# Kernel optimization log

Measured on AMD Instinct MI355X. Metric: run time of the kernel, lower is better.

Reference implementation:

```python
import jax, jax.numpy as jnp
import numpy as np

EPS = 1e-12

def _l2norm(x):
    # F.normalize(p=2, dim=1) with eps clamp on the norm
    n = jnp.linalg.norm(x, axis=1, keepdims=True)
    return x / jnp.maximum(n, EPS)

def _xavier_uniform(key, shape, gain=1.414):
    fan_in, fan_out = shape[-1], shape[0]
    a = gain * np.sqrt(6.0 / (fan_in + fan_out))
    return jax.random.uniform(key, shape, jnp.float32, -a, a)

def setup_inputs() -> dict:
    NUM_ENT, NUM_REL, D, E, B = 100000, 500, 512, 150000, 4096
    key = jax.random.key(0)
    ks = jax.random.split(key, 12)
    heads = jax.random.randint(ks[0], (B, 1), 0, NUM_ENT)
    rels  = jax.random.randint(ks[1], (B, 1), 0, NUM_REL)
    tails = jax.random.randint(ks[2], (B, 1), 0, NUM_ENT)
    triples = jnp.concatenate([heads, rels, tails], axis=1)           # [B,3]
    node_list = jax.random.randint(ks[3], (2, E), 0, NUM_ENT)          # [2,E] (src,dst)
    edge_list = jax.random.randint(ks[4], (E,), 0, NUM_REL)            # [E] relation per edge
    return {
        "triples": triples,
        "node_list": node_list,
        "edge_list": edge_list,
        "ent_emb_init": jax.random.normal(ks[5], (NUM_ENT, D), jnp.float32),
        "rel_emb_init": jax.random.normal(ks[6], (NUM_REL, D), jnp.float32),
        "W_1": _xavier_uniform(ks[7], (D, D)),
        "W_a": _xavier_uniform(ks[8], (1, D)),
        "g_0": _xavier_uniform(ks[9], (1, D)),
        "W_E": _xavier_uniform(ks[10], (D, D)),
        "W_R": _xavier_uniform(ks[11], (D, D)),
    }

def reference(triples, node_list, edge_list, ent_emb_init, rel_emb_init,
              W_1, W_a, g_0, W_E, W_R):
    num_ent = ent_emb_init.shape[0]
    e0 = _l2norm(ent_emb_init)                      # normalized entity table [N,D]
    src, dst = node_list[0], node_list[1]
    h_i = e0[src]                                   # [E,D]
    h_j = e0[dst]                                   # [E,D]
    g_k = rel_emb_init[edge_list]                   # [E,D]

    # c_ijk = W_1 @ (h_j*g_k)^T  -> kept edge-major as [E,D]
    c = (h_j * g_k) @ W_1.T                         # [E,D]
    a = -jax.nn.leaky_relu((h_i * jnp.tanh(c)) @ W_a[0], 0.2)   # [E]
    c_base = (h_i * g_0) @ W_1.T                    # [E,D]
    a_base = -jax.nn.leaky_relu((h_i * jnp.tanh(c_base)) @ W_a[0], 0.2)  # [E]

    a_exp = jnp.exp(a)                              # [E]
    ab_exp = jnp.exp(a_base)                        # [E]

    # segment-softmax denominator: sum of edge exps per source node + baseline term
    a_exp_sum = jax.ops.segment_sum(a_exp[:, None], src, num_segments=num_ent)  # [N,1]
    # baseline exp depends only on src node -> duplicate scatter-set writes identical values
    ab_sorted = jnp.zeros_like(a_exp_sum).at[src].set(ab_exp[:, None])           # [N,1]
    denom = ab_sorted + a_exp_sum
    denom = jnp.where(denom == 0.0, EPS, denom)

    # weighted scatter-aggregate of messages (dropout omitted: eval-mode identity)
    ac = a_exp[:, None] * c                         # [E,D]
    ac_base = ab_exp[:, None] * c_base              # [E,D]
    a_new = jax.ops.segment_sum(ac, src, num_segments=num_ent)                   # [N,D]
    ab_new = jnp.zeros_like(a_new).at[src].set(ac_base)                          # [N,D]

    h_prime = jax.nn.elu((ab_new + a_new) / denom)  # [N,D]
    ent_new = _l2norm(e0 @ W_E + h_prime)           # [N,D]
    rel_new = rel_emb_init @ W_R                    # [R,D]

    head = ent_new[triples[:, 0]][:, None, :]       # [B,1,D]
    rel  = rel_new[triples[:, 1]][:, None, :]       # [B,1,D]
    tail = ent_new[triples[:, 2]][:, None, :]       # [B,1,D]
    return jnp.concatenate([head, rel, tail], axis=1)  # [B,3,D]
```

## Files before the change

### kernel.cpp

```cpp
#include <hip/hip_runtime.h>
#include <cmath>


#define DDIM 512
#define MAXM 65536
#define GBM 128
#define GBN 128

typedef __attribute__((ext_vector_type(8))) short short8;
typedef __attribute__((ext_vector_type(4))) short short4v;
typedef __attribute__((ext_vector_type(4))) float fv4;
typedef unsigned short u16;
typedef unsigned long long u64;

#define LOG2E 1.4426950408889634f

__device__ __forceinline__ float fast_tanh(float x) {
    x = fminf(fmaxf(x, -30.f), 30.f);
    float e = __builtin_amdgcn_exp2f(2.f * LOG2E * x);
    return (e - 1.f) * __builtin_amdgcn_rcpf(e + 1.f);
}
__device__ __forceinline__ float fast_elu(float x) {
    return x > 0.f ? x : (__builtin_amdgcn_exp2f(LOG2E * x) - 1.f);
}
__device__ __forceinline__ float sexp(float x) {
    float lr = x >= 0.f ? x : 0.2f * x;
    return expf(-lr);
}
__device__ __forceinline__ u16 f2bf(float x) {
    unsigned u = __float_as_uint(x);
    u += 0x7FFFu + ((u >> 16) & 1u);
    return (u16)(u >> 16);
}
__device__ __forceinline__ float bf2f(u16 h) {
    return __uint_as_float((unsigned)h << 16);
}
__device__ __forceinline__ void cvt8(const float* v, short8& h8, short8& l8) {
    #pragma unroll
    for (int i = 0; i < 8; i++) {
        u16 h = f2bf(v[i]);
        h8[i] = (short)h;
        l8[i] = (short)f2bf(v[i] - bf2f(h));
    }
}
__device__ __forceinline__ void gld16(const void* g, void* l) {
    __builtin_amdgcn_global_load_lds(
        (const __attribute__((address_space(1))) unsigned int*)g,
        (__attribute__((address_space(3))) unsigned int*)l,
        16, 0, 0);
}

__global__ void hist_kernel(const int* __restrict__ src, int* __restrict__ cnt, int E)
{
    int e = blockIdx.x * 256 + threadIdx.x;
    if (e < E) atomicAdd(&cnt[src[e]], 1);
}

__global__ __launch_bounds__(1024)
void scan_lookback_kernel(const int* __restrict__ in, int* __restrict__ out,
                          int* __restrict__ out2, int n,
                          int* __restrict__ ticket, u64* __restrict__ state)
{
    __shared__ int sh[1024];
    __shared__ int bidSh, exSh;
    int t = threadIdx.x;
    if (t == 0) bidSh = atomicAdd(ticket, 1);
    __syncthreads();
    int bid = bidSh;
    int i = bid * 1024 + t;
    int v = (i < n) ? in[i] : 0;
    sh[t] = v;
    __syncthreads();
    for (int o = 1; o < 1024; o <<= 1) {
        int x = (t >= o) ? sh[t - o] : 0;
        __syncthreads();
        sh[t] += x;
        __syncthreads();
    }
    int incl = sh[t];
    int agg = sh[1023];
    if (t == 0) {
        u64 pub = (bid == 0) ? ((2ull << 32) | (unsigned)agg)
                             : ((1ull << 32) | (unsigned)agg);
        __hip_atomic_store(&state[bid], pub, __ATOMIC_RELEASE, __HIP_MEMORY_SCOPE_AGENT);
        int ex = 0;
        if (bid > 0) {
            int p = bid - 1;
            for (;;) {
                u64 s;
                do {
                    s = __hip_atomic_load(&state[p], __ATOMIC_ACQUIRE, __HIP_MEMORY_SCOPE_AGENT);
                } while ((s >> 32) == 0);
                ex += (int)(unsigned)s;
                if ((s >> 32) == 2ull) break;
                p--;
            }
            __hip_atomic_store(&state[bid], (2ull << 32) | (unsigned)(ex + agg),
                               __ATOMIC_RELEASE, __HIP_MEMORY_SCOPE_AGENT);
        }
        exSh = ex;
    }
    __syncthreads();
    int ex = exSh;
    if (i < n) {
        int e = ex + incl - v;
        out[i] = e;
        if (out2) out2[i] = e;
        if (i == n - 1) out[n] = ex + incl;
    }
}

__global__ __launch_bounds__(1024)
void scan_small_kernel(const int* __restrict__ in, int* __restrict__ out, int n)
{
    __shared__ int wsum[16];
    __shared__ int carrySh;
    int t = threadIdx.x, lane = t & 63, w = t >> 6;
    if (t == 0) carrySh = 0;
    __syncthreads();
    for (int base = 0; base < n; base += 1024) {
        int i = base + t;
        int v = (i < n) ? in[i] : 0;
        int s = v;
        #pragma unroll
        for (int o = 1; o < 64; o <<= 1) {
            int x = __shfl_up(s, o);
            if (lane >= o) s += x;
        }
        if (lane == 63) wsum[w] = s;
        __syncthreads();
        int wo = 0;
        for (int k = 0; k < w; k++) wo += wsum[k];
        int carry = carrySh;
        if (i < n) out[i] = carry + wo + s - v;
        __syncthreads();
        if (t == 1023) carrySh = carry + wo + s;
        __syncthreads();
    }
    if (t == 0) out[n] = carrySh;
}

__global__ void bucket_slotdeg_kernel(const int* __restrict__ src, int* __restrict__ cursor,
                                      int* __restrict__ edge_ids, int E,
                                      const int* __restrict__ triples, const int* __restrict__ rowSt,
                                      int* __restrict__ slotNode, int* __restrict__ deg, int NS)
{
    int i = blockIdx.x * 256 + threadIdx.x;
    if (i < E) { int p = atomicAdd(&cursor[src[i]], 1); edge_ids[p] = i; }
    int r = i - E;
    if (r >= 0 && r < NS) {
        int b = r >> 1, p = (r & 1) * 2;
        int n = triples[b * 3 + p];
        slotNode[r] = n;
        deg[r] = rowSt[n + 1] - rowSt[n];
    }
}

__global__ void fill_rows_kernel(const int* __restrict__ slotNode, const int* __restrict__ rowSt,
                                 const int* __restrict__ edgeIds, const int* __restrict__ slotOff,
                                 int* __restrict__ rows, int* __restrict__ srcL, int NS)
{
    int r = blockIdx.x * 256 + threadIdx.x;
    if (r >= NS) return;
    int n = slotNode[r];
    int gs = rowSt[n], d = rowSt[n + 1] - gs, mo = slotOff[r];
    for (int j = 0; j < d && mo + j < MAXM; j++) {
        rows[mo + j] = edgeIds[gs + j];
        srcL[mo + j] = n;
    }
}


__global__ __launch_bounds__(256)
void wfrag_kernel(const float* __restrict__ W1, const float* __restrict__ WE,
                  const float* __restrict__ WR, const float* __restrict__ relEmb,
                  int R,
                  u16* __restrict__ W1H, u16* __restrict__ W1L,
                  u16* __restrict__ WEH, u16* __restrict__ WEL,
                  u16* __restrict__ WRH, u16* __restrict__ WRL,
                  u16* __restrict__ ArH, u16* __restrict__ ArL)
{
    int mat = blockIdx.y;
    const float* src = (mat == 0) ? W1 : (mat == 1) ? WE : (mat == 2) ? WR : relEmb;
    u16* hi = (mat == 0) ? W1H : (mat == 1) ? WEH : (mat == 2) ? WRH : ArH;
    u16* lo = (mat == 0) ? W1L : (mat == 1) ? WEL : (mat == 2) ? WRL : ArL;
    bool tr = (mat == 1 || mat == 2);
    int rows = (mat == 3) ? R : DDIM;

    int nt = ((rows + 127) >> 7) << 3;
    int wid = threadIdx.x >> 6, lane = threadIdx.x & 63;
    int l15 = lane & 15, seg = (lane >> 4) * 8;
    for (int rt = blockIdx.x * 4 + wid; rt < nt; rt += gridDim.x * 4) {
        int r = min(rt * 16 + l15, rows - 1);
        size_t base = (size_t)rt * 8192 + (size_t)lane * 8;
        #pragma unroll 2
        for (int kt = 0; kt < 16; kt++) {
            float v[8];
            if (!tr) {
                const float* p = src + (size_t)r * DDIM + seg + kt * 32;
                float4 x0 = *(const float4*)p;
                float4 x1 = *(const float4*)(p + 4);
                v[0]=x0.x; v[1]=x0.y; v[2]=x0.z; v[3]=x0.w;
                v[4]=x1.x; v[5]=x1.y; v[6]=x1.z; v[7]=x1.w;
            } else {
                int k0 = kt * 32 + seg;
                #pragma unroll
                for (int i = 0; i < 8; i++)
                    v[i] = src[(size_t)(k0 + i) * DDIM + r];
            }
            short8 h8, l8; cvt8(v, h8, l8);
            *(short8*)(hi + base + (size_t)kt * 512) = h8;
            *(short8*)(lo + base + (size_t)kt * 512) = l8;
        }
    }
}

__global__ __launch_bounds__(256)
void afrag_es_kernel(const float* __restrict__ entEmb, float* __restrict__ invN,
                     const float* __restrict__ relEmb, const float* __restrict__ g0,
                     const int* __restrict__ rowsL, const int* __restrict__ dstIdx,
                     const int* __restrict__ relIdx, const int* __restrict__ slotNode,
                     const int* __restrict__ Mdev, int NS,
                     u16* __restrict__ AeH, u16* __restrict__ AeL,
                     u16* __restrict__ As1H, u16* __restrict__ As1L,
                     u16* __restrict__ As3H, u16* __restrict__ As3L)
{
    int M = max(1, min(MAXM, *Mdev));
    int ntE = ((M + 127) >> 7) << 3;
    int ntS = ((NS + 127) >> 7) << 3;
    int total = ntE + ntS;
    int wid = threadIdx.x >> 6, lane = threadIdx.x & 63;
    int l15 = lane & 15, seg = (lane >> 4) * 8;

    for (int g = blockIdx.x * 4 + wid; g < total; g += gridDim.x * 4) {
        bool isE = g < ntE;
        int rt = isE ? g : g - ntE;
        int node, rl = 0;
        if (isE) {
            int m = min(rt * 16 + l15, M - 1);
            int e = rowsL[m];
            node = dstIdx[e]; rl = relIdx[e];
        } else {
            node = slotNode[min(rt * 16 + l15, NS - 1)];
        }
        const float* ep = entEmb + (size_t)node * DDIM + seg;
        float ss = 0.f;
        for (int kt = 0; kt < 16; kt++) {
            float4 x0 = *(const float4*)(ep + kt * 32);
            float4 x1 = *(const float4*)(ep + kt * 32 + 4);
            ss += x0.x*x0.x + x0.y*x0.y + x0.z*x0.z + x0.w*x0.w
                + x1.x*x1.x + x1.y*x1.y + x1.z*x1.z + x1.w*x1.w;
        }
        ss += __shfl_xor(ss, 16);
        ss += __shfl_xor(ss, 32);
        float sc = 1.f / fmaxf(sqrtf(ss), 1e-12f);
        if (lane < 16) invN[node] = sc;
        size_t base = (size_t)rt * 8192 + (size_t)lane * 8;
        if (isE) {
            const float* rp = relEmb + (size_t)rl * DDIM + seg;
            #pragma unroll 4
            for (int kt = 0; kt < 16; kt++) {
                float4 x0 = *(const float4*)(ep + kt * 32);
                float4 x1 = *(const float4*)(ep + kt * 32 + 4);
                float4 y0 = *(const float4*)(rp + kt * 32);
                float4 y1 = *(const float4*)(rp + kt * 32 + 4);
                float v[8] = {sc*x0.x*y0.x, sc*x0.y*y0.y, sc*x0.z*y0.z, sc*x0.w*y0.w,
                              sc*x1.x*y1.x, sc*x1.y*y1.y, sc*x1.z*y1.z, sc*x1.w*y1.w};
                short8 h8, l8; cvt8(v, h8, l8);
                *(short8*)(AeH + base + (size_t)kt * 512) = h8;
                *(short8*)(AeL + base + (size_t)kt * 512) = l8;
            }
        } else {
            const float* gp = g0 + seg;
            #pragma unroll 2
            for (int kt = 0; kt < 16; kt++) {
                float4 x0 = *(const float4*)(ep + kt * 32);
                float4 x1 = *(const float4*)(ep + kt * 32 + 4);
                float4 y0 = *(const float4*)(gp + kt * 32);
                float4 y1 = *(const float4*)(gp + kt * 32 + 4);
                float v3[8] = {sc*x0.x, sc*x0.y, sc*x0.z, sc*x0.w,
                               sc*x1.x, sc*x1.y, sc*x1.z, sc*x1.w};
                float v1[8] = {v3[0]*y0.x, v3[1]*y0.y, v3[2]*y0.z, v3[3]*y0.w,
                               v3[4]*y1.x, v3[5]*y1.y, v3[6]*y1.z, v3[7]*y1.w};
                short8 h8, l8;
                cvt8(v3, h8, l8);
                *(short8*)(As3H + base + (size_t)kt * 512) = h8;
                *(short8*)(As3L + base + (size_t)kt * 512) = l8;
                cvt8(v1, h8, l8);
                *(short8*)(As1H + base + (size_t)kt * 512) = h8;
                *(short8*)(As1L + base + (size_t)kt * 512) = l8;
            }
        }
    }
}

__global__ __launch_bounds__(256, 2)
void gemm_score_k(const u16* __restrict__ AeH, const u16* __restrict__ AeL,
                  const u16* __restrict__ As1H, const u16* __restrict__ As1L,
                  const u16* __restrict__ W1H, const u16* __restrict__ W1L,
                  const float* __restrict__ entEmb, const float* __restrict__ invNorm,
                  const int* __restrict__ srcL, const int* __restrict__ slotNode,
                  const float* __restrict__ Wa, float* __restrict__ scoreP,
                  const int* __restrict__ Mdev, int NS, int SCLEN)
{
    __shared__ __align__(1024) u16 lds[2][32 * 512];
    int M = max(1, min(MAXM, *Mdev));
    int TE = (M + 127) >> 7, TS = (NS + 127) >> 7;
    int total = TE + TS;
    int lane = threadIdx.x & 63, wid = threadIdx.x >> 6;
    int waveM = wid >> 1, waveN = wid & 1;
    int quad = lane >> 4, l15 = lane & 15;
    int n0 = blockIdx.y * GBN;
    int ldsChunk0 = wid * 8;

    for (int tt = blockIdx.x; tt < total; tt += gridDim.x) {
        bool isE = tt < TE;
        int m0 = (isE ? tt : tt - TE) * GBM;
        int Mt = isE ? M : NS;
        const u16* g1 = isE
            ? ((wid == 0) ? AeH : (wid == 1) ? AeL : (wid == 2) ? W1H : W1L)
            : ((wid == 0) ? As1H : (wid == 1) ? As1L : (wid == 2) ? W1H : W1L);
        int rowBase = (wid < 2) ? (m0 >> 4) : (n0 >> 4);
        const u16* s1 = g1 + (size_t)rowBase * 8192 + (size_t)lane * 8;

        fv4 acc[4][4];
        #pragma unroll
        for (int i = 0; i < 4; i++)
            #pragma unroll
            for (int j = 0; j < 4; j++) acc[i][j] = fv4{0.f, 0.f, 0.f, 0.f};

        int cur = 0;
        #pragma unroll
        for (int q = 0; q < 8; q++)
            gld16(s1 + (size_t)q * 8192, &lds[0][(ldsChunk0 + q) * 512]);
        __syncthreads();

        for (int kk = 0; kk < 16; kk++) {
            if (kk < 15) {
                size_t go = (size_t)(kk + 1) * 512;
                #pragma unroll
                for (int q = 0; q < 8; q++)
                    gld16(s1 + (size_t)q * 8192 + go,
                          &lds[cur ^ 1][(ldsChunk0 + q) * 512]);
            }
            const u16* buf = &lds[cur][0];
            short8 aH[4], aL[4], bH[4], bL[4];
            #pragma unroll
            for (int i = 0; i < 4; i++) {
                aH[i] = *(const short8*)&buf[(waveM * 4 + i) * 512 + lane * 8];
                aL[i] = *(const short8*)&buf[(8 + waveM * 4 + i) * 512 + lane * 8];
                bH[i] = *(const short8*)&buf[(16 + waveN * 4 + i) * 512 + lane * 8];
                bL[i] = *(const short8*)&buf[(24 + waveN * 4 + i) * 512 + lane * 8];
            }
            #pragma unroll
            for (int i = 0; i < 4; i++)
                #pragma unroll
                for (int j = 0; j < 4; j++) {
                    acc[i][j] = __builtin_amdgcn_mfma_f32_16x16x32_bf16(aH[i], bH[j], acc[i][j], 0, 0, 0);
                    acc[i][j] = __builtin_amdgcn_mfma_f32_16x16x32_bf16(aH[i], bL[j], acc[i][j], 0, 0, 0);
                    acc[i][j] = __builtin_amdgcn_mfma_f32_16x16x32_bf16(aL[i], bH[j], acc[i][j], 0, 0, 0);
                }
            __syncthreads();
            cur ^= 1;
        }

        int base = isE ? 0 : MAXM;
        #pragma unroll
        for (int i = 0; i < 4; i++) {
            #pragma unroll
            for (int reg = 0; reg < 4; reg++) {
                int gm = m0 + waveM * 64 + i * 16 + quad * 4 + reg;
                bool valid = gm < Mt;
                int gmc = valid ? gm : 0;
                int srcn = isE ? srcL[gmc] : slotNode[gmc];
                float invs = invNorm[srcn];
                float s = 0.f;
                #pragma unroll
                for (int j = 0; j < 4; j++) {
                    int col = n0 + waveN * 64 + j * 16 + l15;
                    float hv = entEmb[(size_t)srcn * DDIM + col];
                    float wv = Wa[col];
                    s += fast_tanh(acc[i][j][reg]) * hv * wv;
                }
                s *= invs;
                s += __shfl_xor(s, 8); s += __shfl_xor(s, 4);
                s += __shfl_xor(s, 2); s += __shfl_xor(s, 1);
                if (l15 == 0 && valid)
                    scoreP[(size_t)blockIdx.y * SCLEN + base + gm] = s;
            }
        }
    }
}

__global__ __launch_bounds__(256, 2)
void gemm_tail_k(const u16* __restrict__ ApH, const u16* __restrict__ ApL,
                 const u16* __restrict__ W1H, const u16* __restrict__ W1L,
                 const u16* __restrict__ As3H, const u16* __restrict__ As3L,
                 const u16* __restrict__ WEH, const u16* __restrict__ WEL,
                 const u16* __restrict__ ArH, const u16* __restrict__ ArL,
                 const u16* __restrict__ WRH, const u16* __restrict__ WRL,
                 const float* __restrict__ invDenom,
                 float* __restrict__ ENT, float* __restrict__ relnew, int NS, int R)
{
    __shared__ __align__(1024) u16 lds[2][32 * 512];
    int lane = threadIdx.x & 63, wid = threadIdx.x >> 6;
    int waveM = wid >> 1, waveN = wid & 1;
    int quad = lane >> 4, l15 = lane & 15;
    int n0 = blockIdx.y * GBN;
    int TS = (NS + 127) >> 7, TR = (R + 127) >> 7;
    int total = TS + TR;
    int ldsChunk0 = wid * 8;

    for (int tt = blockIdx.x; tt < total; tt += gridDim.x) {
        bool fused = tt < TS;
        int m0 = (fused ? tt : tt - TS) * GBM;
        int Mt = fused ? NS : R;
        float* Cout = fused ? ENT : relnew;
        const u16* g1 = fused
            ? ((wid == 0) ? ApH : (wid == 1) ? ApL : (wid == 2) ? W1H : W1L)
            : ((wid == 0) ? ArH : (wid == 1) ? ArL : (wid == 2) ? WRH : WRL);
        const u16* g2 = fused
            ? ((wid == 0) ? As3H : (wid == 1) ? As3L : (wid == 2) ? WEH : WEL)
            : nullptr;
        int nkk = fused ? 32 : 16;
        int rowBase = (wid < 2) ? (m0 >> 4) : (n0 >> 4);
        const u16* s1 = g1 + (size_t)rowBase * 8192 + (size_t)lane * 8;
        const u16* s2 = fused ? g2 + (size_t)rowBase * 8192 + (size_t)lane * 8 : nullptr;

        fv4 acc[4][4];
        #pragma unroll
        for (int i = 0; i < 4; i++)
            #pragma unroll
            for (int j = 0; j < 4; j++) acc[i][j] = fv4{0.f, 0.f, 0.f, 0.f};

        int cur = 0;
        #pragma unroll
        for (int q = 0; q < 8; q++)
            gld16(s1 + (size_t)q * 8192, &lds[0][(ldsChunk0 + q) * 512]);
        __syncthreads();

        for (int kk = 0; kk < nkk; kk++) {
            int kn = kk + 1;
            if (kn < nkk) {
                const u16* sp = (fused && kn >= 16) ? s2 : s1;
                size_t go = (size_t)(kn & 15) * 512;
                #pragma unroll
                for (int q = 0; q < 8; q++)
                    gld16(sp + (size_t)q * 8192 + go,
                          &lds[cur ^ 1][(ldsChunk0 + q) * 512]);
            }
            const u16* buf = &lds[cur][0];
            short8 aH[4], aL[4], bH[4], bL[4];
            #pragma unroll
            for (int i = 0; i < 4; i++) {
                aH[i] = *(const short8*)&buf[(waveM * 4 + i) * 512 + lane * 8];
                aL[i] = *(const short8*)&buf[(8 + waveM * 4 + i) * 512 + lane * 8];
                bH[i] = *(const short8*)&buf[(16 + waveN * 4 + i) * 512 + lane * 8];
                bL[i] = *(const short8*)&buf[(24 + waveN * 4 + i) * 512 + lane * 8];
            }
            #pragma unroll
            for (int i = 0; i < 4; i++)
                #pragma unroll
                for (int j = 0; j < 4; j++) {
                    acc[i][j] = __builtin_amdgcn_mfma_f32_16x16x32_bf16(aH[i], bH[j], acc[i][j], 0, 0, 0);
                    acc[i][j] = __builtin_amdgcn_mfma_f32_16x16x32_bf16(aH[i], bL[j], acc[i][j], 0, 0, 0);
                    acc[i][j] = __builtin_amdgcn_mfma_f32_16x16x32_bf16(aL[i], bH[j], acc[i][j], 0, 0, 0);
                }
            if (fused && kk == 15) {
                #pragma unroll
                for (int i = 0; i < 4; i++)
                    #pragma unroll
                    for (int reg = 0; reg < 4; reg++) {
                        int gm = m0 + waveM * 64 + i * 16 + quad * 4 + reg;
                        float idv = invDenom[min(gm, Mt - 1)];
                        #pragma unroll
                        for (int j = 0; j < 4; j++)
                            acc[i][j][reg] = fast_elu(acc[i][j][reg] * idv);
                    }
            }
            __syncthreads();
            cur ^= 1;
        }

        #pragma unroll
        for (int i = 0; i < 4; i++) {
            #pragma unroll
            for (int reg = 0; reg < 4; reg++) {
                int gm = m0 + waveM * 64 + i * 16 + quad * 4 + reg;
                if (gm >= Mt) continue;
                #pragma unroll
                for (int j = 0; j < 4; j++) {
                    int col = n0 + waveN * 64 + j * 16 + l15;
                    Cout[(size_t)gm * DDIM + col] = acc[i][j][reg];
                }
            }
        }
    }
}

__global__ __launch_bounds__(128)
void build_p_kernel(const int* __restrict__ deg, const int* __restrict__ slotOff,
                    const float* __restrict__ scoreP, int SCLEN, int NS,
                    const u16* __restrict__ AeH, const u16* __restrict__ AeL,
                    const u16* __restrict__ As1H, const u16* __restrict__ As1L,
                    u16* __restrict__ ApH, u16* __restrict__ ApL,
                    float* __restrict__ invDenom)
{
    int r = blockIdx.x, t = threadIdx.x;
    int kt = t >> 3;
    int qsel = (t >> 1) & 3;
    int j0 = (t & 1) * 4;
    size_t ktoff = (size_t)kt * 512 + j0;
    float a0 = 0.f, a1 = 0.f, a2 = 0.f, a3 = 0.f;
    float dInv = 1.f;
    if (r < NS) {
        int d = deg[r];
        if (d > 0) {
            int mo = slotOff[r];
            int si = MAXM + r;
            float ab = sexp(scoreP[si] + scoreP[SCLEN + si]
                          + scoreP[2 * SCLEN + si] + scoreP[3 * SCLEN + si]);
            size_t so = (size_t)(r >> 4) * 8192 + ktoff + (size_t)((r & 15) + 16 * qsel) * 8;
            short4v h4 = *(const short4v*)(As1H + so);
            short4v l4 = *(const short4v*)(As1L + so);
            a0 = ab * (bf2f((u16)h4[0]) + bf2f((u16)l4[0]));
            a1 = ab * (bf2f((u16)h4[1]) + bf2f((u16)l4[1]));
            a2 = ab * (bf2f((u16)h4[2]) + bf2f((u16)l4[2]));
            a3 = ab * (bf2f((u16)h4[3]) + bf2f((u16)l4[3]));
            float denom = ab;
            for (int j = 0; j < d; j++) {
                int ei = mo + j;
                if (ei >= MAXM) break;
                float ae = sexp(scoreP[ei] + scoreP[SCLEN + ei]
                              + scoreP[2 * SCLEN + ei] + scoreP[3 * SCLEN + ei]);
                size_t eo = (size_t)(ei >> 4) * 8192 + ktoff + (size_t)((ei & 15) + 16 * qsel) * 8;
                short4v eh = *(const short4v*)(AeH + eo);
                short4v el = *(const short4v*)(AeL + eo);
                a0 = fmaf(ae, bf2f((u16)eh[0]) + bf2f((u16)el[0]), a0);
                a1 = fmaf(ae, bf2f((u16)eh[1]) + bf2f((u16)el[1]), a1);
                a2 = fmaf(ae, bf2f((u16)eh[2]) + bf2f((u16)el[2]), a2);
                a3 = fmaf(ae, bf2f((u16)eh[3]) + bf2f((u16)el[3]), a3);
                denom += ae;
            }
            dInv = 1.f / denom;
        }
    }
    size_t fo = (size_t)(r >> 4) * 8192 + ktoff + (size_t)((r & 15) + 16 * qsel) * 8;
    float v[4] = {a0, a1, a2, a3};
    short4v h4, l4;
    #pragma unroll
    for (int i = 0; i < 4; i++) {
        u16 h = f2bf(v[i]);
        h4[i] = (short)h;
        l4[i] = (short)f2bf(v[i] - bf2f(h));
    }
    *(short4v*)(ApH + fo) = h4;
    *(short4v*)(ApL + fo) = l4;
    if (t == 0 && r < NS) invDenom[r] = dInv;
}

__global__ __launch_bounds__(128)
void gather_out_kernel(const int* __restrict__ triples, const float* __restrict__ ENT,
                       const float* __restrict__ relnew, float* __restrict__ out)
{
    int r = blockIdx.x;
    int b = r / 3, j = r - b * 3;
    int t = threadIdx.x;
    size_t oo = (size_t)r * DDIM + t * 4;
    if (j == 1) {
        const float* srow = relnew + (size_t)triples[r] * DDIM;
        *(float4*)(out + oo) = *(const float4*)(srow + t * 4);
        return;
    }
    const float* srow = ENT + (size_t)(b * 2 + (j == 2 ? 1 : 0)) * DDIM;
    float4 v = *(const float4*)(srow + t * 4);
    float s = v.x*v.x + v.y*v.y + v.z*v.z + v.w*v.w;
    #pragma unroll
    for (int off = 32; off > 0; off >>= 1) s += __shfl_down(s, off);
    __shared__ float ws2[2];
    if ((t & 63) == 0) ws2[t >> 6] = s;
    __syncthreads();
    float inv = 1.f / fmaxf(sqrtf(ws2[0] + ws2[1]), 1e-12f);
    *(float4*)(out + oo) = make_float4(v.x*inv, v.y*inv, v.z*inv, v.w*inv);
}

extern "C" void kernel_launch(void* const* d_in, const int* in_sizes, int n_in,
                              void* d_out, int out_size, void* d_ws, size_t ws_size,
                              hipStream_t stream)
{
    const int*   triples = (const int*)  d_in[0];
    const int*   nodes   = (const int*)  d_in[1];
    const int*   edges   = (const int*)  d_in[2];
    const float* entEmb  = (const float*)d_in[3];
    const float* relEmb  = (const float*)d_in[4];
    const float* W1      = (const float*)d_in[5];
    const float* Wa      = (const float*)d_in[6];
    const float* g0      = (const float*)d_in[7];
    const float* WE      = (const float*)d_in[8];
    const float* WR      = (const float*)d_in[9];

    const int B  = in_sizes[0] / 3;
    const int E  = in_sizes[2];
    const int N  = in_sizes[3] / DDIM;
    const int R  = in_sizes[4] / DDIM;
    const int NS = 2 * B;
    const int* srcIdx = nodes;
    const int* dstIdx = nodes + E;

    char* ws = (char*)d_ws;
    size_t off = 0;
    auto carve = [&](size_t bytes) -> void* {
        void* p = ws + off;
        off = (off + bytes + 255) & ~(size_t)255;
        return p;
    };
    const int NS128 = ((NS + 127) / 128) * 128;
    const int R128  = ((R + 127) / 128) * 128;
    const int SCLEN = MAXM + NS128;
    float* ENT      = (float*)carve((size_t)NS * DDIM * 4);
    float* relnew   = (float*)carve((size_t)R * DDIM * 4);
    float* invNorm  = (float*)carve((size_t)N * 4);
    float* scoreP   = (float*)carve((size_t)4 * SCLEN * 4);
    float* invDen   = (float*)carve((size_t)NS * 4);
    char*  zbase    = ws + off;
    int*   cnt      = (int*)carve((size_t)N * 4);
    int*   ticket   = (int*)carve(256);
    u64*   stateN   = (u64*)carve((size_t)1024 * 8);
    size_t zbytes   = (size_t)((ws + off) - zbase);
    int*   rowSt    = (int*)carve((size_t)(N + 1) * 4);
    int*   cursor   = (int*)carve((size_t)N * 4);
    int*   edgeIds  = (int*)carve((size_t)E * 4);
    int*   slotNode = (int*)carve((size_t)NS * 4);
    int*   deg      = (int*)carve((size_t)NS * 4);
    int*   slotOff  = (int*)carve((size_t)(NS + 1) * 4);
    int*   rowsL    = (int*)carve((size_t)MAXM * 4);
    int*   srcL     = (int*)carve((size_t)MAXM * 4);
    u16* AeH  = (u16*)carve((size_t)MAXM * DDIM * 2);
    u16* AeL  = (u16*)carve((size_t)MAXM * DDIM * 2);
    u16* As1H = (u16*)carve((size_t)NS128 * DDIM * 2);
    u16* As1L = (u16*)carve((size_t)NS128 * DDIM * 2);
    u16* As3H = (u16*)carve((size_t)NS128 * DDIM * 2);
    u16* As3L = (u16*)carve((size_t)NS128 * DDIM * 2);
    u16* ApH  = (u16*)carve((size_t)NS128 * DDIM * 2);
    u16* ApL  = (u16*)carve((size_t)NS128 * DDIM * 2);
    u16* ArH  = (u16*)carve((size_t)R128 * DDIM * 2);
    u16* ArL  = (u16*)carve((size_t)R128 * DDIM * 2);
    u16* W1H  = (u16*)carve((size_t)DDIM * DDIM * 2);
    u16* W1L  = (u16*)carve((size_t)DDIM * DDIM * 2);
    u16* WEH  = (u16*)carve((size_t)DDIM * DDIM * 2);
    u16* WEL  = (u16*)carve((size_t)DDIM * DDIM * 2);
    u16* WRH  = (u16*)carve((size_t)DDIM * DDIM * 2);
    u16* WRL  = (u16*)carve((size_t)DDIM * DDIM * 2);
    (void)ws_size; (void)n_in; (void)out_size;

    hipMemsetAsync(zbase, 0, zbytes, stream);
    hist_kernel<<<(E + 255) / 256, 256, 0, stream>>>(srcIdx, cnt, E);
    scan_lookback_kernel<<<(N + 1023) / 1024, 1024, 0, stream>>>(
        cnt, rowSt, cursor, N, ticket, stateN);
    bucket_slotdeg_kernel<<<(E + NS + 255) / 256, 256, 0, stream>>>(
        srcIdx, cursor, edgeIds, E, triples, rowSt, slotNode, deg, NS);
    scan_small_kernel<<<1, 1024, 0, stream>>>(deg, slotOff, NS);
    const int* Mdev = slotOff + NS;
    fill_rows_kernel<<<(NS + 255) / 256, 256, 0, stream>>>(slotNode, rowSt, edgeIds,
                                                           slotOff, rowsL, srcL, NS);
    wfrag_kernel<<<dim3(8, 4), 256, 0, stream>>>(W1, WE, WR, relEmb, R,
                                                 W1H, W1L, WEH, WEL, WRH, WRL, ArH, ArL);
    afrag_es_kernel<<<256, 256, 0, stream>>>(entEmb, invNorm, relEmb, g0,
                                             rowsL, dstIdx, edges, slotNode,
                                             Mdev, NS,
                                             AeH, AeL, As1H, As1L, As3H, As3L);
    gemm_score_k<<<dim3(192, DDIM / GBN), 256, 0, stream>>>(
        AeH, AeL, As1H, As1L, W1H, W1L, entEmb, invNorm, srcL, slotNode,
        Wa, scoreP, Mdev, NS, SCLEN);
    build_p_kernel<<<NS128, 128, 0, stream>>>(deg, slotOff, scoreP, SCLEN, NS,
                                              AeH, AeL, As1H, As1L,
                                              ApH, ApL, invDen);
    int gTail = ((NS + GBM - 1) / GBM) + ((R + GBM - 1) / GBM);
    gemm_tail_k<<<dim3(gTail, DDIM / GBN), 256, 0, stream>>>(
        ApH, ApL, W1H, W1L, As3H, As3L, WEH, WEL, ArH, ArL, WRH, WRL,
        invDen, ENT, relnew, NS, R);
    gather_out_kernel<<<B * 3, 128, 0, stream>>>(triples, ENT, relnew, (float*)d_out);
}
```

Before: 503.1 us.

## Fold g_0 into W1 fragments and fuse histogram with weight conversion

The baseline gating vector g_0 is folded into a pre-scaled copy of W1 (W1*g0), so the slot-row A operand no longer needs its own g0-multiplied split-bf16 buffer. The As1 buffers disappear, and the score GEMM and build_p reuse As3, with build_p applying g0 on the fly. The histogram and weight-fragment kernels are merged into one launch, and afrag caches the entity row in registers instead of loading it twice. The score GEMM grid drops from 192 to 128 blocks, and the larger register footprint in afrag could lower its occupancy.

Result: no change. 507.2 us (+0.8%).

```diff
diff --git a/kernel.cpp b/kernel.cpp
--- a/kernel.cpp
+++ b/kernel.cpp
@@ -50,10 +50,67 @@
         16, 0, 0);
 }
 
-__global__ void hist_kernel(const int* __restrict__ src, int* __restrict__ cnt, int E)
-{
-    int e = blockIdx.x * 256 + threadIdx.x;
-    if (e < E) atomicAdd(&cnt[src[e]], 1);
+
+__global__ __launch_bounds__(256)
+void hist_wfrag_kernel(const int* __restrict__ src, int* __restrict__ cnt, int E, int HB,
+                       const float* __restrict__ W1, const float* __restrict__ WE,
+                       const float* __restrict__ WR, const float* __restrict__ relEmb,
+                       const float* __restrict__ g0, int R,
+                       u16* __restrict__ W1H, u16* __restrict__ W1L,
+                       u16* __restrict__ W1GH, u16* __restrict__ W1GL,
+                       u16* __restrict__ WEH, u16* __restrict__ WEL,
+                       u16* __restrict__ WRH, u16* __restrict__ WRL,
+                       u16* __restrict__ ArH, u16* __restrict__ ArL)
+{
+    if (blockIdx.x < (unsigned)HB) {
+        int e = blockIdx.x * 256 + threadIdx.x;
+        if (e < E) atomicAdd(&cnt[src[e]], 1);
+        return;
+    }
+    int wb = blockIdx.x - HB;
+    int mat = wb >> 3, bx = wb & 7;
+    const float* srcM = (mat == 0) ? W1 : (mat == 1) ? WE : (mat == 2) ? WR : relEmb;
+    u16* hi = (mat == 0) ? W1H : (mat == 1) ? WEH : (mat == 2) ? WRH : ArH;
+    u16* lo = (mat == 0) ? W1L : (mat == 1) ? WEL : (mat == 2) ? WRL : ArL;
+    bool tr = (mat == 1 || mat == 2);
+    int rows = (mat == 3) ? R : DDIM;
+
+    int nt = ((rows + 127) >> 7) << 3;
+    int wid = threadIdx.x >> 6, lane = threadIdx.x & 63;
+    int l15 = lane & 15, seg = (lane >> 4) * 8;
+    for (int rt = bx * 4 + wid; rt < nt; rt += 32) {
+        int r = min(rt * 16 + l15, rows - 1);
+        size_t base = (size_t)rt * 8192 + (size_t)lane * 8;
+        #pragma unroll 2
+        for (int kt = 0; kt < 16; kt++) {
+            float v[8];
+            if (!tr) {
+                const float* p = srcM + (size_t)r * DDIM + seg + kt * 32;
+                float4 x0 = *(const float4*)p;
+                float4 x1 = *(const float4*)(p + 4);
+                v[0]=x0.x; v[1]=x0.y; v[2]=x0.z; v[3]=x0.w;
+                v[4]=x1.x; v[5]=x1.y; v[6]=x1.z; v[7]=x1.w;
+            } else {
+                int k0 = kt * 32 + seg;
+                #pragma unroll
+                for (int i = 0; i < 8; i++)
+                    v[i] = srcM[(size_t)(k0 + i) * DDIM + r];
+            }
+            short8 h8, l8; cvt8(v, h8, l8);
+            *(short8*)(hi + base + (size_t)kt * 512) = h8;
+            *(short8*)(lo + base + (size_t)kt * 512) = l8;
+            if (mat == 0) {
+                const float* gp = g0 + seg + kt * 32;
+                float4 g0a = *(const float4*)gp;
+                float4 g0b = *(const float4*)(gp + 4);
+                float v2[8] = {v[0]*g0a.x, v[1]*g0a.y, v[2]*g0a.z, v[3]*g0a.w,
+                               v[4]*g0b.x, v[5]*g0b.y, v[6]*g0b.z, v[7]*g0b.w};
+                cvt8(v2, h8, l8);
+                *(short8*)(W1GH + base + (size_t)kt * 512) = h8;
+                *(short8*)(W1GL + base + (size_t)kt * 512) = l8;
+            }
+        }
+    }
 }
 
 __global__ __launch_bounds__(1024)
@@ -170,59 +227,13 @@
     }
 }
 
-
-__global__ __launch_bounds__(256)
-void wfrag_kernel(const float* __restrict__ W1, const float* __restrict__ WE,
-                  const float* __restrict__ WR, const float* __restrict__ relEmb,
-                  int R,
-                  u16* __restrict__ W1H, u16* __restrict__ W1L,
-                  u16* __restrict__ WEH, u16* __restrict__ WEL,
-                  u16* __restrict__ WRH, u16* __restrict__ WRL,
-                  u16* __restrict__ ArH, u16* __restrict__ ArL)
-{
-    int mat = blockIdx.y;
-    const float* src = (mat == 0) ? W1 : (mat == 1) ? WE : (mat == 2) ? WR : relEmb;
-    u16* hi = (mat == 0) ? W1H : (mat == 1) ? WEH : (mat == 2) ? WRH : ArH;
-    u16* lo = (mat == 0) ? W1L : (mat == 1) ? WEL : (mat == 2) ? WRL : ArL;
-    bool tr = (mat == 1 || mat == 2);
-    int rows = (mat == 3) ? R : DDIM;
-
-    int nt = ((rows + 127) >> 7) << 3;
-    int wid = threadIdx.x >> 6, lane = threadIdx.x & 63;
-    int l15 = lane & 15, seg = (lane >> 4) * 8;
-    for (int rt = blockIdx.x * 4 + wid; rt < nt; rt += gridDim.x * 4) {
-        int r = min(rt * 16 + l15, rows - 1);
-        size_t base = (size_t)rt * 8192 + (size_t)lane * 8;
-        #pragma unroll 2
-        for (int kt = 0; kt < 16; kt++) {
-            float v[8];
-            if (!tr) {
-                const float* p = src + (size_t)r * DDIM + seg + kt * 32;
-                float4 x0 = *(const float4*)p;
-                float4 x1 = *(const float4*)(p + 4);
-                v[0]=x0.x; v[1]=x0.y; v[2]=x0.z; v[3]=x0.w;
-                v[4]=x1.x; v[5]=x1.y; v[6]=x1.z; v[7]=x1.w;
-            } else {
-                int k0 = kt * 32 + seg;
-                #pragma unroll
-                for (int i = 0; i < 8; i++)
-                    v[i] = src[(size_t)(k0 + i) * DDIM + r];
-            }
-            short8 h8, l8; cvt8(v, h8, l8);
-            *(short8*)(hi + base + (size_t)kt * 512) = h8;
-            *(short8*)(lo + base + (size_t)kt * 512) = l8;
-        }
-    }
-}
-
 __global__ __launch_bounds__(256)
 void afrag_es_kernel(const float* __restrict__ entEmb, float* __restrict__ invN,
-                     const float* __restrict__ relEmb, const float* __restrict__ g0,
+                     const float* __restrict__ relEmb,
                      const int* __restrict__ rowsL, const int* __restrict__ dstIdx,
                      const int* __restrict__ relIdx, const int* __restrict__ slotNode,
                      const int* __restrict__ Mdev, int NS,
                      u16* __restrict__ AeH, u16* __restrict__ AeL,
-                     u16* __restrict__ As1H, u16* __restrict__ As1L,
                      u16* __restrict__ As3H, u16* __restrict__ As3L)
 {
     int M = max(1, min(MAXM, *Mdev));
@@ -244,10 +255,14 @@
             node = slotNode[min(rt * 16 + l15, NS - 1)];
         }
         const float* ep = entEmb + (size_t)node * DDIM + seg;
+        float row[16][8];
         float ss = 0.f;
+        #pragma unroll
         for (int kt = 0; kt < 16; kt++) {
             float4 x0 = *(const float4*)(ep + kt * 32);
             float4 x1 = *(const float4*)(ep + kt * 32 + 4);
+            row[kt][0]=x0.x; row[kt][1]=x0.y; row[kt][2]=x0.z; row[kt][3]=x0.w;
+            row[kt][4]=x1.x; row[kt][5]=x1.y; row[kt][6]=x1.z; row[kt][7]=x1.w;
             ss += x0.x*x0.x + x0.y*x0.y + x0.z*x0.z + x0.w*x0.w
                 + x1.x*x1.x + x1.y*x1.y + x1.z*x1.z + x1.w*x1.w;
         }
@@ -258,37 +273,26 @@
         size_t base = (size_t)rt * 8192 + (size_t)lane * 8;
         if (isE) {
             const float* rp = relEmb + (size_t)rl * DDIM + seg;
-            #pragma unroll 4
+            #pragma unroll
             for (int kt = 0; kt < 16; kt++) {
-                float4 x0 = *(const float4*)(ep + kt * 32);
-                float4 x1 = *(const float4*)(ep + kt * 32 + 4);
                 float4 y0 = *(const float4*)(rp + kt * 32);
                 float4 y1 = *(const float4*)(rp + kt * 32 + 4);
-                float v[8] = {sc*x0.x*y0.x, sc*x0.y*y0.y, sc*x0.z*y0.z, sc*x0.w*y0.w,
-                              sc*x1.x*y1.x, sc*x1.y*y1.y, sc*x1.z*y1.z, sc*x1.w*y1.w};
+                float v[8] = {sc*row[kt][0]*y0.x, sc*row[kt][1]*y0.y,
+                              sc*row[kt][2]*y0.z, sc*row[kt][3]*y0.w,
+                              sc*row[kt][4]*y1.x, sc*row[kt][5]*y1.y,
+                              sc*row[kt][6]*y1.z, sc*row[kt][7]*y1.w};
                 short8 h8, l8; cvt8(v, h8, l8);
                 *(short8*)(AeH + base + (size_t)kt * 512) = h8;
                 *(short8*)(AeL + base + (size_t)kt * 512) = l8;
             }
         } else {
-            const float* gp = g0 + seg;
-            #pragma unroll 2
+            #pragma unroll
             for (int kt = 0; kt < 16; kt++) {
-                float4 x0 = *(const float4*)(ep + kt * 32);
-                float4 x1 = *(const float4*)(ep + kt * 32 + 4);
-                float4 y0 = *(const float4*)(gp + kt * 32);
-                float4 y1 = *(const float4*)(gp + kt * 32 + 4);
-                float v3[8] = {sc*x0.x, sc*x0.y, sc*x0.z, sc*x0.w,
-                               sc*x1.x, sc*x1.y, sc*x1.z, sc*x1.w};
-                float v1[8] = {v3[0]*y0.x, v3[1]*y0.y, v3[2]*y0.z, v3[3]*y0.w,
-                               v3[4]*y1.x, v3[5]*y1.y, v3[6]*y1.z, v3[7]*y1.w};
-                short8 h8, l8;
-                cvt8(v3, h8, l8);
+                float v[8] = {sc*row[kt][0], sc*row[kt][1], sc*row[kt][2], sc*row[kt][3],
+                              sc*row[kt][4], sc*row[kt][5], sc*row[kt][6], sc*row[kt][7]};
+                short8 h8, l8; cvt8(v, h8, l8);
                 *(short8*)(As3H + base + (size_t)kt * 512) = h8;
                 *(short8*)(As3L + base + (size_t)kt * 512) = l8;
-                cvt8(v1, h8, l8);
-                *(short8*)(As1H + base + (size_t)kt * 512) = h8;
-                *(short8*)(As1L + base + (size_t)kt * 512) = l8;
             }
         }
     }
@@ -296,8 +300,9 @@
 
 __global__ __launch_bounds__(256, 2)
 void gemm_score_k(const u16* __restrict__ AeH, const u16* __restrict__ AeL,
-                  const u16* __restrict__ As1H, const u16* __restrict__ As1L,
+                  const u16* __restrict__ As3H, const u16* __restrict__ As3L,
                   const u16* __restrict__ W1H, const u16* __restrict__ W1L,
+                  const u16* __restrict__ W1GH, const u16* __restrict__ W1GL,
                   const float* __restrict__ entEmb, const float* __restrict__ invNorm,
                   const int* __restrict__ srcL, const int* __restrict__ slotNode,
                   const float* __restrict__ Wa, float* __restrict__ scoreP,
@@ -319,7 +324,7 @@
         int Mt = isE ? M : NS;
         const u16* g1 = isE
             ? ((wid == 0) ? AeH : (wid == 1) ? AeL : (wid == 2) ? W1H : W1L)
-            : ((wid == 0) ? As1H : (wid == 1) ? As1L : (wid == 2) ? W1H : W1L);
+            : ((wid == 0) ? As3H : (wid == 1) ? As3L : (wid == 2) ? W1GH : W1GL);
         int rowBase = (wid < 2) ? (m0 >> 4) : (n0 >> 4);
         const u16* s1 = g1 + (size_t)rowBase * 8192 + (size_t)lane * 8;
 
@@ -502,7 +507,8 @@
 void build_p_kernel(const int* __restrict__ deg, const int* __restrict__ slotOff,
                     const float* __restrict__ scoreP, int SCLEN, int NS,
                     const u16* __restrict__ AeH, const u16* __restrict__ AeL,
-                    const u16* __restrict__ As1H, const u16* __restrict__ As1L,
+                    const u16* __restrict__ As3H, const u16* __restrict__ As3L,
+                    const float* __restrict__ g0,
                     u16* __restrict__ ApH, u16* __restrict__ ApL,
                     float* __restrict__ invDenom)
 {
@@ -521,12 +527,13 @@
             float ab = sexp(scoreP[si] + scoreP[SCLEN + si]
                           + scoreP[2 * SCLEN + si] + scoreP[3 * SCLEN + si]);
             size_t so = (size_t)(r >> 4) * 8192 + ktoff + (size_t)((r & 15) + 16 * qsel) * 8;
-            short4v h4 = *(const short4v*)(As1H + so);
-            short4v l4 = *(const short4v*)(As1L + so);
-            a0 = ab * (bf2f((u16)h4[0]) + bf2f((u16)l4[0]));
-            a1 = ab * (bf2f((u16)h4[1]) + bf2f((u16)l4[1]));
-            a2 = ab * (bf2f((u16)h4[2]) + bf2f((u16)l4[2]));
-            a3 = ab * (bf2f((u16)h4[3]) + bf2f((u16)l4[3]));
+            short4v h4 = *(const short4v*)(As3H + so);
+            short4v l4 = *(const short4v*)(As3L + so);
+            float4 gv = *(const float4*)(g0 + t * 4);
+            a0 = ab * gv.x * (bf2f((u16)h4[0]) + bf2f((u16)l4[0]));
+            a1 = ab * gv.y * (bf2f((u16)h4[1]) + bf2f((u16)l4[1]));
+            a2 = ab * gv.z * (bf2f((u16)h4[2]) + bf2f((u16)l4[2]));
+            a3 = ab * gv.w * (bf2f((u16)h4[3]) + bf2f((u16)l4[3]));
             float denom = ab;
             for (int j = 0; j < d; j++) {
                 int ei = mo + j;
@@ -637,8 +644,6 @@
     int*   srcL     = (int*)carve((size_t)MAXM * 4);
     u16* AeH  = (u16*)carve((size_t)MAXM * DDIM * 2);
     u16* AeL  = (u16*)carve((size_t)MAXM * DDIM * 2);
-    u16* As1H = (u16*)carve((size_t)NS128 * DDIM * 2);
-    u16* As1L = (u16*)carve((size_t)NS128 * DDIM * 2);
     u16* As3H = (u16*)carve((size_t)NS128 * DDIM * 2);
     u16* As3L = (u16*)carve((size_t)NS128 * DDIM * 2);
     u16* ApH  = (u16*)carve((size_t)NS128 * DDIM * 2);
@@ -647,6 +652,8 @@
     u16* ArL  = (u16*)carve((size_t)R128 * DDIM * 2);
     u16* W1H  = (u16*)carve((size_t)DDIM * DDIM * 2);
     u16* W1L  = (u16*)carve((size_t)DDIM * DDIM * 2);
+    u16* W1GH = (u16*)carve((size_t)DDIM * DDIM * 2);
+    u16* W1GL = (u16*)carve((size_t)DDIM * DDIM * 2);
     u16* WEH  = (u16*)carve((size_t)DDIM * DDIM * 2);
     u16* WEL  = (u16*)carve((size_t)DDIM * DDIM * 2);
     u16* WRH  = (u16*)carve((size_t)DDIM * DDIM * 2);
@@ -654,7 +661,10 @@
     (void)ws_size; (void)n_in; (void)out_size;
 
     hipMemsetAsync(zbase, 0, zbytes, stream);
-    hist_kernel<<<(E + 255) / 256, 256, 0, stream>>>(srcIdx, cnt, E);
+    int HB = (E + 255) / 256;
+    hist_wfrag_kernel<<<HB + 32, 256, 0, stream>>>(
+        srcIdx, cnt, E, HB, W1, WE, WR, relEmb, g0, R,
+        W1H, W1L, W1GH, W1GL, WEH, WEL, WRH, WRL, ArH, ArL);
     scan_lookback_kernel<<<(N + 1023) / 1024, 1024, 0, stream>>>(
         cnt, rowSt, cursor, N, ticket, stateN);
     bucket_slotdeg_kernel<<<(E + NS + 255) / 256, 256, 0, stream>>>(
@@ -663,17 +673,15 @@
     const int* Mdev = slotOff + NS;
     fill_rows_kernel<<<(NS + 255) / 256, 256, 0, stream>>>(slotNode, rowSt, edgeIds,
                                                            slotOff, rowsL, srcL, NS);
-    wfrag_kernel<<<dim3(8, 4), 256, 0, stream>>>(W1, WE, WR, relEmb, R,
-                                                 W1H, W1L, WEH, WEL, WRH, WRL, ArH, ArL);
-    afrag_es_kernel<<<256, 256, 0, stream>>>(entEmb, invNorm, relEmb, g0,
+    afrag_es_kernel<<<256, 256, 0, stream>>>(entEmb, invNorm, relEmb,
                                              rowsL, dstIdx, edges, slotNode,
                                              Mdev, NS,
-                                             AeH, AeL, As1H, As1L, As3H, As3L);
-    gemm_score_k<<<dim3(192, DDIM / GBN), 256, 0, stream>>>(
-        AeH, AeL, As1H, As1L, W1H, W1L, entEmb, invNorm, srcL, slotNode,
-        Wa, scoreP, Mdev, NS, SCLEN);
+                                             AeH, AeL, As3H, As3L);
+    gemm_score_k<<<dim3(128, DDIM / GBN), 256, 0, stream>>>(
+        AeH, AeL, As3H, As3L, W1H, W1L, W1GH, W1GL,
+        entEmb, invNorm, srcL, slotNode, Wa, scoreP, Mdev, NS, SCLEN);
     build_p_kernel<<<NS128, 128, 0, stream>>>(deg, slotOff, scoreP, SCLEN, NS,
-                                              AeH, AeL, As1H, As1L,
+                                              AeH, AeL, As3H, As3L, g0,
                                               ApH, ApL, invDen);
     int gTail = ((NS + GBM - 1) / GBM) + ((R + GBM - 1) / GBM);
     gemm_tail_k<<<dim3(gTail, DDIM / GBN), 256, 0, stream>>>(
```
